# Optimization experiments

Hardware: AMD Instinct MI355X
Metric: run time of the kernel (lower is better)

The kernel has to match this reference:

```python
import jax, jax.numpy as jnp
import numpy as np

GRID = 20            # grid_size -> n1 = 400 nodes
CTX = 64             # context_size
HID = 10 * CTX       # hidden_dim per module code
BATCH = 256
K_ITERS = 100        # Dykstra iterations approximating the exact QP solve
LEAKY_SLOPE = 0.1


def _grid_incidence(g):
    """Incidence matrix of g x g grid DAG with right/down edges (SPO benchmark)."""
    n1 = g * g
    edges = []
    for i in range(g):
        for j in range(g):
            u = i * g + j
            if j + 1 < g:
                edges.append((u, u + 1))   # right
            if i + 1 < g:
                edges.append((u, u + g))   # down
    n2 = len(edges)
    A = np.zeros((n1, n2), dtype=np.float32)
    for e, (u, v) in enumerate(edges):
        A[u, e] = 1.0    # flow leaves u
        A[v, e] = -1.0   # flow enters v
    b = np.zeros(n1, dtype=np.float32)
    b[0] = 1.0           # source
    b[-1] = -1.0         # sink
    return A, b


def setup_inputs() -> dict:
    key = jax.random.key(0)
    ks = jax.random.split(key, 5)
    A_np, b_np = _grid_incidence(GRID)
    n2 = A_np.shape[1]
    d = jax.random.normal(ks[0], (BATCH, CTX), dtype=jnp.float32)
    W1 = jax.random.normal(ks[1], (CTX, HID), dtype=jnp.float32) / np.sqrt(CTX)
    b1 = jax.random.normal(ks[2], (HID,), dtype=jnp.float32) * 0.01
    W2 = jax.random.normal(ks[3], (HID, n2), dtype=jnp.float32) / np.sqrt(HID)
    b2 = jax.random.normal(ks[4], (n2,), dtype=jnp.float32) * 0.01
    return {
        "d": d, "W1": W1, "b1": b1, "W2": W2, "b2": b2,
        "A": jnp.asarray(A_np), "b_eq": jnp.asarray(b_np),
    }


def _solve_qp(w, A, b_eq):
    """Batched min_x w'x + 0.5||x||^2 s.t. Ax=b, x>=0 == proj of -w onto the
    feasible set, via Dykstra alternating projections (affine set / orthant)."""
    M = jnp.linalg.pinv(A @ A.T)  # [n1, n1]; AA' is the grid Laplacian (rank n1-1)

    def proj_affine(x):           # x: [B, n2]
        resid = x @ A.T - b_eq    # [B, n1]
        return x - (resid @ M) @ A

    y0 = -w                       # point to project
    p0 = jnp.zeros_like(w)
    q0 = jnp.zeros_like(w)

    def step(carry, _):
        y, p, q = carry
        t = y + p
        yp = proj_affine(t)
        p = t - yp
        t2 = yp + q
        y = jnp.maximum(t2, 0.0)  # projection onto x >= 0
        q = t2 - y
        return (y, p, q), None

    (y, _, _), _ = jax.lax.scan(step, (y0, p0, q0), None, length=K_ITERS)
    return y


def reference(d, W1, b1, W2, b2, A, b_eq):
    h = d @ W1 + b1
    h = jnp.where(h > 0, h, LEAKY_SLOPE * h)   # LeakyReLU(0.1)
    w = h @ W2 + b2                            # predicted edge costs [B, n2]
    return _solve_qp(w, A, b_eq)               # training-mode output: QP solution
```

## Files before the change

### kernel.cpp

```cpp
#include <hip/hip_runtime.h>
#include <math.h>

#define G 20
#define N1 400
#define N2 760
#define CTXS 64
#define HID 640
#define NB 256
#define ITERS 100
#define PI_F 3.14159265358979323846f

__device__ __forceinline__ int eR(int i, int j) { return (i < 19) ? (39 * i + 2 * j) : (741 + j); }
__device__ __forceinline__ int eD(int i, int j) { return (j < 19) ? (39 * i + 2 * j + 1) : (39 * i + 38); }

#define LOAD_ROW20(dst, base) do {                                          \
    const float4* _rp = (const float4*)(base);                              \
    float4 _r0 = _rp[0], _r1 = _rp[1], _r2 = _rp[2], _r3 = _rp[3], _r4 = _rp[4]; \
    dst[0]=_r0.x; dst[1]=_r0.y; dst[2]=_r0.z; dst[3]=_r0.w;                 \
    dst[4]=_r1.x; dst[5]=_r1.y; dst[6]=_r1.z; dst[7]=_r1.w;                 \
    dst[8]=_r2.x; dst[9]=_r2.y; dst[10]=_r2.z; dst[11]=_r2.w;               \
    dst[12]=_r3.x; dst[13]=_r3.y; dst[14]=_r3.z; dst[15]=_r3.w;             \
    dst[16]=_r4.x; dst[17]=_r4.y; dst[18]=_r4.z; dst[19]=_r4.w; } while (0)

__global__ __launch_bounds__(256, 1) void spnet_kernel(
    const float* __restrict__ dmat, const float* __restrict__ W1,
    const float* __restrict__ b1v, const float* __restrict__ W2,
    const float* __restrict__ b2v, float* __restrict__ out)
{
  const int tid = threadIdx.x;
  const int bb  = blockIdx.x;

  __shared__ __align__(16) float sdrow[CTXS];
  __shared__ __align__(16) float sh[HID];
  __shared__ __align__(16) float st0[N2];
  __shared__ __align__(16) float srowT[N1];
  __shared__ __align__(16) float sc1[N1];
  __shared__ __align__(16) float sc2T[N1];
  __shared__ __align__(16) float sd1[N1];
  __shared__ __align__(16) float szz[N1];
  __shared__ __align__(16) float tRs[G][G];
  __shared__ __align__(16) float tDs[21][G];

  for (int t = tid; t < N1; t += 256) ((float*)tRs)[t] = 0.f;
  for (int t = tid; t < 21 * G; t += 256) ((float*)tDs)[t] = 0.f;
  if (tid < CTXS) sdrow[tid] = dmat[bb * CTXS + tid];

  const bool isC = (tid < 200);
  const int c  = tid / 10;
  const int u  = tid % 10;
  const int k0 = 2 * u;

  float VA0[10], VA1[10], VC[20], S0, S1;
  {
    const float n0 = 0.22360679774997896f, nk = 0.31622776601683794f;
#pragma unroll
    for (int i = 0; i < 10; ++i) {
      VA0[i] = ((k0 == 0) ? n0 : nk) * cosf((float)(k0 * (2 * i + 1)) * (PI_F / 40.f));
      VA1[i] = nk * cosf((float)((k0 + 1) * (2 * i + 1)) * (PI_F / 40.f));
    }
#pragma unroll
    for (int k = 0; k < 20; ++k)
      VC[k] = ((k == 0) ? n0 : nk) * cosf((float)(k * (2 * u + 1)) * (PI_F / 40.f));
    float lc = 2.f - 2.f * cosf((float)c * (PI_F / 20.f));
    float l0 = 2.f - 2.f * cosf((float)k0 * (PI_F / 20.f));
    float l1 = 2.f - 2.f * cosf((float)(k0 + 1) * (PI_F / 20.f));
    S0 = (c == 0 && k0 == 0) ? 0.f : 1.f / (lc + l0);
    S1 = 1.f / (lc + l1);
  }

  __syncthreads();

  if (tid < HID / 4) {
    float4 acc = *(const float4*)(b1v + 4 * tid);
#pragma unroll 4
    for (int k = 0; k < CTXS; k += 4) {
      float4 h4 = *(const float4*)(sdrow + k);
      const float* wb = W1 + k * HID + 4 * tid;
      float4 w0 = *(const float4*)(wb);
      float4 w1 = *(const float4*)(wb + HID);
      float4 w2 = *(const float4*)(wb + 2 * HID);
      float4 w3 = *(const float4*)(wb + 3 * HID);
      acc.x = fmaf(h4.x, w0.x, acc.x); acc.y = fmaf(h4.x, w0.y, acc.y);
      acc.z = fmaf(h4.x, w0.z, acc.z); acc.w = fmaf(h4.x, w0.w, acc.w);
      acc.x = fmaf(h4.y, w1.x, acc.x); acc.y = fmaf(h4.y, w1.y, acc.y);
      acc.z = fmaf(h4.y, w1.z, acc.z); acc.w = fmaf(h4.y, w1.w, acc.w);
      acc.x = fmaf(h4.z, w2.x, acc.x); acc.y = fmaf(h4.z, w2.y, acc.y);
      acc.z = fmaf(h4.z, w2.z, acc.z); acc.w = fmaf(h4.z, w2.w, acc.w);
      acc.x = fmaf(h4.w, w3.x, acc.x); acc.y = fmaf(h4.w, w3.y, acc.y);
      acc.z = fmaf(h4.w, w3.z, acc.z); acc.w = fmaf(h4.w, w3.w, acc.w);
    }
    acc.x = acc.x > 0.f ? acc.x : 0.1f * acc.x;
    acc.y = acc.y > 0.f ? acc.y : 0.1f * acc.y;
    acc.z = acc.z > 0.f ? acc.z : 0.1f * acc.z;
    acc.w = acc.w > 0.f ? acc.w : 0.1f * acc.w;
    *(float4*)(sh + 4 * tid) = acc;
  }
  __syncthreads();

  if (tid < N2 / 4) {
    float4 acc = *(const float4*)(b2v + 4 * tid);
#pragma unroll 2
    for (int k = 0; k < HID; k += 4) {
      float4 h4 = *(const float4*)(sh + k);
      const float* wb = W2 + k * N2 + 4 * tid;
      float4 w0 = *(const float4*)(wb);
      float4 w1 = *(const float4*)(wb + N2);
      float4 w2 = *(const float4*)(wb + 2 * N2);
      float4 w3 = *(const float4*)(wb + 3 * N2);
      acc.x = fmaf(h4.x, w0.x, acc.x); acc.y = fmaf(h4.x, w0.y, acc.y);
      acc.z = fmaf(h4.x, w0.z, acc.z); acc.w = fmaf(h4.x, w0.w, acc.w);
      acc.x = fmaf(h4.y, w1.x, acc.x); acc.y = fmaf(h4.y, w1.y, acc.y);
      acc.z = fmaf(h4.y, w1.z, acc.z); acc.w = fmaf(h4.y, w1.w, acc.w);
      acc.x = fmaf(h4.z, w2.x, acc.x); acc.y = fmaf(h4.z, w2.y, acc.y);
      acc.z = fmaf(h4.z, w2.z, acc.z); acc.w = fmaf(h4.z, w2.w, acc.w);
      acc.x = fmaf(h4.w, w3.x, acc.x); acc.y = fmaf(h4.w, w3.y, acc.y);
      acc.z = fmaf(h4.w, w3.z, acc.z); acc.w = fmaf(h4.w, w3.w, acc.w);
    }
    float4 s; s.x = -acc.x; s.y = -acc.y; s.z = -acc.z; s.w = -acc.w;
    *(float4*)(st0 + 4 * tid) = s;
  }

  const int  di = tid / 5, dj4 = (tid % 5) * 4;
  const bool dAct = (tid < 100) && (di < 19);
  float dT[4], dQ[4], dY[4];
  const int  rid = tid - 128;
  const bool isR = (rid >= 0 && rid < 100);
  const int  ri = isR ? (rid / 5) : 0, rj4 = isR ? ((rid % 5) * 4) : 0;
  float rT[4], rQ[4], rY[4];
#pragma unroll
  for (int m = 0; m < 4; ++m) { dT[m]=0.f; dQ[m]=0.f; dY[m]=0.f; rT[m]=0.f; rQ[m]=0.f; rY[m]=0.f; }

  __syncthreads();

  if (dAct) {
#pragma unroll
    for (int m = 0; m < 4; ++m) dT[m] = st0[eD(di, dj4 + m)];
    *(float4*)&tDs[di + 1][dj4] = make_float4(dT[0], dT[1], dT[2], dT[3]);
  }
  if (isR) {
#pragma unroll
    for (int m = 0; m < 4; ++m) {
      int j = rj4 + m;
      rT[m] = (j < 19) ? st0[eR(ri, j)] : 0.f;
    }
    *(float4*)&tRs[ri][rj4] = make_float4(rT[0], rT[1], rT[2], rT[3]);
  }
  __syncthreads();

  for (int it = 0; it < ITERS; ++it) {
    if (isR) {
      float4 oR = *(const float4*)&tRs[ri][rj4];
      float  lf = (rj4 > 0) ? tRs[ri][rj4 - 1] : 0.f;
      float4 oD = *(const float4*)&tDs[ri + 1][rj4];
      float4 iD = *(const float4*)&tDs[ri][rj4];
      float r0 = oR.x + oD.x - lf   - iD.x;
      float r1 = oR.y + oD.y - oR.x - iD.y;
      float r2 = oR.z + oD.z - oR.y - iD.z;
      float r3 = oR.w + oD.w - oR.z - iD.w;
      if (ri == 0  && rj4 == 0)  r0 -= 1.f;
      if (ri == 19 && rj4 == 16) r3 += 1.f;
      srowT[(rj4 + 0) * G + ri] = r0;
      srowT[(rj4 + 1) * G + ri] = r1;
      srowT[(rj4 + 2) * G + ri] = r2;
      srowT[(rj4 + 3) * G + ri] = r3;
    }
    __syncthreads();

    if (isC) {
      float d_[20]; LOAD_ROW20(d_, srowT + 20 * c);
      float a0 = 0.f, a1 = 0.f;
#pragma unroll
      for (int i = 0; i < 10; ++i) {
        float e_ = d_[i] + d_[19 - i], o_ = d_[i] - d_[19 - i];
        a0 = fmaf(VA0[i], e_, a0);
        a1 = fmaf(VA1[i], o_, a1);
      }
      sc1[k0 * G + c] = a0;
      sc1[(k0 + 1) * G + c] = a1;
    }
    __syncthreads();

    if (isC) {
      float d_[20]; LOAD_ROW20(d_, sc1 + 20 * c);
      float a0 = 0.f, a1 = 0.f;
#pragma unroll
      for (int j = 0; j < 10; ++j) {
        float e_ = d_[j] + d_[19 - j], o_ = d_[j] - d_[19 - j];
        a0 = fmaf(VA0[j], e_, a0);
        a1 = fmaf(VA1[j], o_, a1);
      }
      sc2T[k0 * G + c] = a0 * S0;
      sc2T[(k0 + 1) * G + c] = a1 * S1;
    }
    __syncthreads();

    if (isC) {
      float d_[20]; LOAD_ROW20(d_, sc2T + 20 * c);
      float E = 0.f, O = 0.f;
#pragma unroll
      for (int m = 0; m < 10; ++m) {
        E = fmaf(VC[2 * m], d_[2 * m], E);
        O = fmaf(VC[2 * m + 1], d_[2 * m + 1], O);
      }
      sd1[u * G + c] = E + O;
      sd1[(19 - u) * G + c] = E - O;
    }
    __syncthreads();

    if (isC) {
      float d_[20]; LOAD_ROW20(d_, sd1 + 20 * c);
      float E = 0.f, O = 0.f;
#pragma unroll
      for (int m = 0; m < 10; ++m) {
        E = fmaf(VC[2 * m], d_[2 * m], E);
        O = fmaf(VC[2 * m + 1], d_[2 * m + 1], O);
      }
      szz[c * G + u] = E + O;
      szz[c * G + (19 - u)] = E - O;
    }
    __syncthreads();

    if (isR) {
      float4 z4 = *(const float4*)&szz[ri * G + rj4];
      float  zR = (rj4 < 16) ? szz[ri * G + rj4 + 4] : 0.f;
      float pn[4] = {z4.x - z4.y, z4.y - z4.z, z4.z - z4.w, z4.w - zR};
      if (rj4 == 16) pn[3] = 0.f;
#pragma unroll
      for (int m = 0; m < 4; ++m) {
        float t2 = rT[m] - pn[m] + rQ[m];
        float yn = fmaxf(t2, 0.f);
        rQ[m] = t2 - yn; rY[m] = yn; rT[m] = yn + pn[m];
      }
      *(float4*)&tRs[ri][rj4] = make_float4(rT[0], rT[1], rT[2], rT[3]);
    }
    if (dAct) {
      float4 z4 = *(const float4*)&szz[di * G + dj4];
      float4 zb = *(const float4*)&szz[(di + 1) * G + dj4];
      float pn[4] = {z4.x - zb.x, z4.y - zb.y, z4.z - zb.z, z4.w - zb.w};
#pragma unroll
      for (int m = 0; m < 4; ++m) {
        float t2 = dT[m] - pn[m] + dQ[m];
        float yn = fmaxf(t2, 0.f);
        dQ[m] = t2 - yn; dY[m] = yn; dT[m] = yn + pn[m];
      }
      *(float4*)&tDs[di + 1][dj4] = make_float4(dT[0], dT[1], dT[2], dT[3]);
    }
    __syncthreads();
  }

  float* mine = out + bb * N2;
  if (isR) {
#pragma unroll
    for (int m = 0; m < 4; ++m) {
      int j = rj4 + m;
      if (j < 19) mine[eR(ri, j)] = rY[m];
    }
  }
  if (dAct) {
#pragma unroll
    for (int m = 0; m < 4; ++m) mine[eD(di, dj4 + m)] = dY[m];
  }
}

extern "C" void kernel_launch(void* const* d_in, const int* in_sizes, int n_in,
                              void* d_out, int out_size, void* d_ws, size_t ws_size,
                              hipStream_t stream) {
  const float* d   = (const float*)d_in[0];
  const float* W1  = (const float*)d_in[1];
  const float* b1  = (const float*)d_in[2];
  const float* W2  = (const float*)d_in[3];
  const float* b2  = (const float*)d_in[4];
  float* out = (float*)d_out;
  spnet_kernel<<<NB, 256, 0, stream>>>(d, W1, b1, W2, b2, out);
}
```

Baseline: 214.9 us.

## Run Dykstra loop in a single wavefront without block barriers

Restricts the iterative projection loop to the first 64 threads (one wavefront on AMD) and removes all __syncthreads, relying on lockstep wave execution with compiler memory fences. Each lane now processes multiple DCT and edge-update tasks serially. DCT coefficient tables move from per-thread registers into shared memory. This trades barrier overhead for less parallelism and more per-lane work, and depends on intra-wave LDS ordering for correctness.

After: 332.5 us. +54.7%, slower.

```diff
diff --git a/kernel.cpp b/kernel.cpp
--- a/kernel.cpp
+++ b/kernel.cpp
@@ -21,6 +21,126 @@
     dst[8]=_r2.x; dst[9]=_r2.y; dst[10]=_r2.z; dst[11]=_r2.w;               \
     dst[12]=_r3.x; dst[13]=_r3.y; dst[14]=_r3.z; dst[15]=_r3.w;             \
     dst[16]=_r4.x; dst[17]=_r4.y; dst[18]=_r4.z; dst[19]=_r4.w; } while (0)
+
+#define LOAD_ROW12(dst, base) do {                                          \
+    const float4* _rp = (const float4*)(base);                              \
+    float4 _r0 = _rp[0], _r1 = _rp[1], _r2 = _rp[2];                        \
+    dst[0]=_r0.x; dst[1]=_r0.y; dst[2]=_r0.z; dst[3]=_r0.w;                 \
+    dst[4]=_r1.x; dst[5]=_r1.y; dst[6]=_r1.z; dst[7]=_r1.w;                 \
+    dst[8]=_r2.x; dst[9]=_r2.y; dst[10]=_r2.z; dst[11]=_r2.w; } while (0)
+
+#define FENCE() asm volatile("" ::: "memory")
+
+#define TASK_RESID(ri, rj4) do {                                            \
+    float4 oR = *(const float4*)&tRs[ri][rj4];                              \
+    float  lf = ((rj4) > 0) ? tRs[ri][(rj4) - 1] : 0.f;                     \
+    float4 oD = *(const float4*)&tDs[(ri) + 1][rj4];                        \
+    float4 iD = *(const float4*)&tDs[ri][rj4];                              \
+    float r0 = oR.x + oD.x - lf   - iD.x;                                   \
+    float r1 = oR.y + oD.y - oR.x - iD.y;                                   \
+    float r2 = oR.z + oD.z - oR.y - iD.z;                                   \
+    float r3 = oR.w + oD.w - oR.z - iD.w;                                   \
+    if ((ri) == 0  && (rj4) == 0)  r0 -= 1.f;                               \
+    if ((ri) == 19 && (rj4) == 16) r3 += 1.f;                               \
+    srowT[((rj4) + 0) * G + (ri)] = r0;                                     \
+    srowT[((rj4) + 1) * G + (ri)] = r1;                                     \
+    srowT[((rj4) + 2) * G + (ri)] = r2;                                     \
+    srowT[((rj4) + 3) * G + (ri)] = r3;                                     \
+  } while (0)
+
+#define TASK_A(cc, uu) do {                                                 \
+    float d_[20]; LOAD_ROW20(d_, srowT + 20 * (cc));                        \
+    float e0_[12]; LOAD_ROW12(e0_, &sVA0[uu][0]);                           \
+    float e1_[12]; LOAD_ROW12(e1_, &sVA1[uu][0]);                           \
+    float a0 = 0.f, a1 = 0.f;                                               \
+    _Pragma("unroll")                                                       \
+    for (int i = 0; i < 10; ++i) {                                          \
+      float e_ = d_[i] + d_[19 - i], o_ = d_[i] - d_[19 - i];               \
+      a0 = fmaf(e0_[i], e_, a0);                                            \
+      a1 = fmaf(e1_[i], o_, a1);                                            \
+    }                                                                       \
+    sc1[(2 * (uu)) * G + (cc)] = a0;                                        \
+    sc1[(2 * (uu) + 1) * G + (cc)] = a1;                                    \
+  } while (0)
+
+#define TASK_B(cc, uu, S0v, S1v) do {                                       \
+    float d_[20]; LOAD_ROW20(d_, sc1 + 20 * (cc));                          \
+    float e0_[12]; LOAD_ROW12(e0_, &sVA0[uu][0]);                           \
+    float e1_[12]; LOAD_ROW12(e1_, &sVA1[uu][0]);                           \
+    float a0 = 0.f, a1 = 0.f;                                               \
+    _Pragma("unroll")                                                       \
+    for (int j = 0; j < 10; ++j) {                                          \
+      float e_ = d_[j] + d_[19 - j], o_ = d_[j] - d_[19 - j];               \
+      a0 = fmaf(e0_[j], e_, a0);                                            \
+      a1 = fmaf(e1_[j], o_, a1);                                            \
+    }                                                                       \
+    sc2T[(2 * (uu)) * G + (cc)] = a0 * (S0v);                               \
+    sc2T[(2 * (uu) + 1) * G + (cc)] = a1 * (S1v);                           \
+  } while (0)
+
+#define TASK_C(cc, uu) do {                                                 \
+    float d_[20]; LOAD_ROW20(d_, sc2T + 20 * (cc));                         \
+    float vc_[20]; LOAD_ROW20(vc_, &sVC[uu][0]);                            \
+    float E = 0.f, O = 0.f;                                                 \
+    _Pragma("unroll")                                                       \
+    for (int m = 0; m < 10; ++m) {                                          \
+      E = fmaf(vc_[2 * m], d_[2 * m], E);                                   \
+      O = fmaf(vc_[2 * m + 1], d_[2 * m + 1], O);                           \
+    }                                                                       \
+    sd1[(uu) * G + (cc)] = E + O;                                           \
+    sd1[(19 - (uu)) * G + (cc)] = E - O;                                    \
+  } while (0)
+
+#define TASK_D(cc, uu) do {                                                 \
+    float d_[20]; LOAD_ROW20(d_, sd1 + 20 * (cc));                          \
+    float vc_[20]; LOAD_ROW20(vc_, &sVC[uu][0]);                            \
+    float E = 0.f, O = 0.f;                                                 \
+    _Pragma("unroll")                                                       \
+    for (int m = 0; m < 10; ++m) {                                          \
+      E = fmaf(vc_[2 * m], d_[2 * m], E);                                   \
+      O = fmaf(vc_[2 * m + 1], d_[2 * m + 1], O);                           \
+    }                                                                       \
+    szz[(cc) * G + (uu)] = E + O;                                           \
+    szz[(cc) * G + (19 - (uu))] = E - O;                                    \
+  } while (0)
+
+#define TASK_ER(ri, rj4, T, Q, Y) do {                                      \
+    float4 z4 = *(const float4*)&szz[(ri) * G + (rj4)];                     \
+    float  zR = ((rj4) < 16) ? szz[(ri) * G + (rj4) + 4] : 0.f;             \
+    float pn[4];                                                            \
+    pn[0] = z4.x - z4.y; pn[1] = z4.y - z4.z; pn[2] = z4.z - z4.w;          \
+    pn[3] = ((rj4) == 16) ? 0.f : (z4.w - zR);                              \
+    _Pragma("unroll")                                                       \
+    for (int m = 0; m < 4; ++m) {                                           \
+      float t2 = T[m] - pn[m] + Q[m];                                       \
+      float yn = fmaxf(t2, 0.f);                                            \
+      Q[m] = t2 - yn; Y[m] = yn; T[m] = yn + pn[m];                         \
+    }                                                                       \
+    *(float4*)&tRs[ri][rj4] = make_float4(T[0], T[1], T[2], T[3]);          \
+  } while (0)
+
+#define TASK_ED(di, dj4, T, Q, Y) do {                                      \
+    float4 z4 = *(const float4*)&szz[(di) * G + (dj4)];                     \
+    float4 zb = *(const float4*)&szz[((di) + 1) * G + (dj4)];               \
+    float pn[4];                                                            \
+    pn[0] = z4.x - zb.x; pn[1] = z4.y - zb.y;                               \
+    pn[2] = z4.z - zb.z; pn[3] = z4.w - zb.w;                               \
+    _Pragma("unroll")                                                       \
+    for (int m = 0; m < 4; ++m) {                                           \
+      float t2 = T[m] - pn[m] + Q[m];                                       \
+      float yn = fmaxf(t2, 0.f);                                            \
+      Q[m] = t2 - yn; Y[m] = yn; T[m] = yn + pn[m];                         \
+    }                                                                       \
+    *(float4*)&tDs[(di) + 1][dj4] = make_float4(T[0], T[1], T[2], T[3]);    \
+  } while (0)
+
+#define CALC_S(cc, uu, S0v, S1v) do {                                       \
+    float lc = 2.f - 2.f * cosf((float)(cc) * (PI_F / 20.f));               \
+    float l0 = 2.f - 2.f * cosf((float)(2 * (uu)) * (PI_F / 20.f));         \
+    float l1 = 2.f - 2.f * cosf((float)(2 * (uu) + 1) * (PI_F / 20.f));     \
+    S0v = ((cc) == 0 && (uu) == 0) ? 0.f : 1.f / (lc + l0);                 \
+    S1v = 1.f / (lc + l1);                                                  \
+  } while (0)
 
 __global__ __launch_bounds__(256, 1) void spnet_kernel(
     const float* __restrict__ dmat, const float* __restrict__ W1,
@@ -40,34 +160,28 @@
   __shared__ __align__(16) float szz[N1];
   __shared__ __align__(16) float tRs[G][G];
   __shared__ __align__(16) float tDs[21][G];
+  __shared__ __align__(16) float sVA0[10][12];
+  __shared__ __align__(16) float sVA1[10][12];
+  __shared__ __align__(16) float sVC[10][20];
 
   for (int t = tid; t < N1; t += 256) ((float*)tRs)[t] = 0.f;
   for (int t = tid; t < 21 * G; t += 256) ((float*)tDs)[t] = 0.f;
+  const float n0c = 0.22360679774997896f, nkc = 0.31622776601683794f;
+  if (tid < 120) {
+    int u = tid / 12, i = tid % 12;
+    float v0 = 0.f, v1 = 0.f;
+    if (i < 10) {
+      int k0 = 2 * u;
+      v0 = ((k0 == 0) ? n0c : nkc) * cosf((float)(k0 * (2 * i + 1)) * (PI_F / 40.f));
+      v1 = nkc * cosf((float)((k0 + 1) * (2 * i + 1)) * (PI_F / 40.f));
+    }
+    sVA0[u][i] = v0; sVA1[u][i] = v1;
+  }
+  if (tid < 200) {
+    int u = tid / 20, k = tid % 20;
+    sVC[u][k] = ((k == 0) ? n0c : nkc) * cosf((float)(k * (2 * u + 1)) * (PI_F / 40.f));
+  }
   if (tid < CTXS) sdrow[tid] = dmat[bb * CTXS + tid];
-
-  const bool isC = (tid < 200);
-  const int c  = tid / 10;
-  const int u  = tid % 10;
-  const int k0 = 2 * u;
-
-  float VA0[10], VA1[10], VC[20], S0, S1;
-  {
-    const float n0 = 0.22360679774997896f, nk = 0.31622776601683794f;
-#pragma unroll
-    for (int i = 0; i < 10; ++i) {
-      VA0[i] = ((k0 == 0) ? n0 : nk) * cosf((float)(k0 * (2 * i + 1)) * (PI_F / 40.f));
-      VA1[i] = nk * cosf((float)((k0 + 1) * (2 * i + 1)) * (PI_F / 40.f));
-    }
-#pragma unroll
-    for (int k = 0; k < 20; ++k)
-      VC[k] = ((k == 0) ? n0 : nk) * cosf((float)(k * (2 * u + 1)) * (PI_F / 40.f));
-    float lc = 2.f - 2.f * cosf((float)c * (PI_F / 20.f));
-    float l0 = 2.f - 2.f * cosf((float)k0 * (PI_F / 20.f));
-    float l1 = 2.f - 2.f * cosf((float)(k0 + 1) * (PI_F / 20.f));
-    S0 = (c == 0 && k0 == 0) ? 0.f : 1.f / (lc + l0);
-    S1 = 1.f / (lc + l1);
-  }
-
   __syncthreads();
 
   if (tid < HID / 4) {
@@ -119,146 +233,94 @@
     float4 s; s.x = -acc.x; s.y = -acc.y; s.z = -acc.z; s.w = -acc.w;
     *(float4*)(st0 + 4 * tid) = s;
   }
-
-  const int  di = tid / 5, dj4 = (tid % 5) * 4;
-  const bool dAct = (tid < 100) && (di < 19);
-  float dT[4], dQ[4], dY[4];
-  const int  rid = tid - 128;
-  const bool isR = (rid >= 0 && rid < 100);
-  const int  ri = isR ? (rid / 5) : 0, rj4 = isR ? ((rid % 5) * 4) : 0;
-  float rT[4], rQ[4], rY[4];
-#pragma unroll
-  for (int m = 0; m < 4; ++m) { dT[m]=0.f; dQ[m]=0.f; dY[m]=0.f; rT[m]=0.f; rQ[m]=0.f; rY[m]=0.f; }
-
   __syncthreads();
 
-  if (dAct) {
-#pragma unroll
-    for (int m = 0; m < 4; ++m) dT[m] = st0[eD(di, dj4 + m)];
-    *(float4*)&tDs[di + 1][dj4] = make_float4(dT[0], dT[1], dT[2], dT[3]);
-  }
-  if (isR) {
-#pragma unroll
-    for (int m = 0; m < 4; ++m) {
-      int j = rj4 + m;
-      rT[m] = (j < 19) ? st0[eR(ri, j)] : 0.f;
-    }
-    *(float4*)&tRs[ri][rj4] = make_float4(rT[0], rT[1], rT[2], rT[3]);
-  }
-  __syncthreads();
+  if (tid >= 64) return;
+  const int t = tid;
+
+  const int c0 = t / 10,         u0 = t % 10;
+  const int c1 = (t + 64) / 10,  u1 = (t + 64) % 10;
+  const int c2 = (t + 128) / 10, u2 = (t + 128) % 10;
+  const int c3 = (t + 192) / 10, u3 = (t + 192) % 10;
+  const bool a3 = (t < 8);
+  float S0_0, S1_0, S0_1, S1_1, S0_2, S1_2, S0_3, S1_3;
+  CALC_S(c0, u0, S0_0, S1_0);
+  CALC_S(c1, u1, S0_1, S1_1);
+  CALC_S(c2, u2, S0_2, S1_2);
+  CALC_S(c3, u3, S0_3, S1_3);
+
+  const int di0 = t / 5,        dj0 = (t % 5) * 4;
+  const int di1 = (t + 64) / 5, dj1 = ((t + 64) % 5) * 4;
+  const bool dA1 = (t < 31);
+  const int ri0 = t / 5,        rj0 = (t % 5) * 4;
+  const int ri1 = (t + 64) / 5, rj1 = ((t + 64) % 5) * 4;
+  const bool rA1 = (t < 36);
+
+  float dT0[4], dQ0[4], dY0[4], dT1[4], dQ1[4], dY1[4];
+  float rT0[4], rQ0[4], rY0[4], rT1[4], rQ1[4], rY1[4];
+#pragma unroll
+  for (int m = 0; m < 4; ++m) {
+    dT0[m] = 0.f; dQ0[m] = 0.f; dY0[m] = 0.f; dT1[m] = 0.f; dQ1[m] = 0.f; dY1[m] = 0.f;
+    rT0[m] = 0.f; rQ0[m] = 0.f; rY0[m] = 0.f; rT1[m] = 0.f; rQ1[m] = 0.f; rY1[m] = 0.f;
+  }
+
+  {
+#pragma unroll
+    for (int m = 0; m < 4; ++m) dT0[m] = st0[eD(di0, dj0 + m)];
+    *(float4*)&tDs[di0 + 1][dj0] = make_float4(dT0[0], dT0[1], dT0[2], dT0[3]);
+  }
+  if (dA1) {
+#pragma unroll
+    for (int m = 0; m < 4; ++m) dT1[m] = st0[eD(di1, dj1 + m)];
+    *(float4*)&tDs[di1 + 1][dj1] = make_float4(dT1[0], dT1[1], dT1[2], dT1[3]);
+  }
+  {
+#pragma unroll
+    for (int m = 0; m < 4; ++m) { int j = rj0 + m; rT0[m] = (j < 19) ? st0[eR(ri0, j)] : 0.f; }
+    *(float4*)&tRs[ri0][rj0] = make_float4(rT0[0], rT0[1], rT0[2], rT0[3]);
+  }
+  if (rA1) {
+#pragma unroll
+    for (int m = 0; m < 4; ++m) { int j = rj1 + m; rT1[m] = (j < 19) ? st0[eR(ri1, j)] : 0.f; }
+    *(float4*)&tRs[ri1][rj1] = make_float4(rT1[0], rT1[1], rT1[2], rT1[3]);
+  }
+  FENCE();
 
   for (int it = 0; it < ITERS; ++it) {
-    if (isR) {
-      float4 oR = *(const float4*)&tRs[ri][rj4];
-      float  lf = (rj4 > 0) ? tRs[ri][rj4 - 1] : 0.f;
-      float4 oD = *(const float4*)&tDs[ri + 1][rj4];
-      float4 iD = *(const float4*)&tDs[ri][rj4];
-      float r0 = oR.x + oD.x - lf   - iD.x;
-      float r1 = oR.y + oD.y - oR.x - iD.y;
-      float r2 = oR.z + oD.z - oR.y - iD.z;
-      float r3 = oR.w + oD.w - oR.z - iD.w;
-      if (ri == 0  && rj4 == 0)  r0 -= 1.f;
-      if (ri == 19 && rj4 == 16) r3 += 1.f;
-      srowT[(rj4 + 0) * G + ri] = r0;
-      srowT[(rj4 + 1) * G + ri] = r1;
-      srowT[(rj4 + 2) * G + ri] = r2;
-      srowT[(rj4 + 3) * G + ri] = r3;
-    }
-    __syncthreads();
-
-    if (isC) {
-      float d_[20]; LOAD_ROW20(d_, srowT + 20 * c);
-      float a0 = 0.f, a1 = 0.f;
-#pragma unroll
-      for (int i = 0; i < 10; ++i) {
-        float e_ = d_[i] + d_[19 - i], o_ = d_[i] - d_[19 - i];
-        a0 = fmaf(VA0[i], e_, a0);
-        a1 = fmaf(VA1[i], o_, a1);
-      }
-      sc1[k0 * G + c] = a0;
-      sc1[(k0 + 1) * G + c] = a1;
-    }
-    __syncthreads();
-
-    if (isC) {
-      float d_[20]; LOAD_ROW20(d_, sc1 + 20 * c);
-      float a0 = 0.f, a1 = 0.f;
-#pragma unroll
-      for (int j = 0; j < 10; ++j) {
-        float e_ = d_[j] + d_[19 - j], o_ = d_[j] - d_[19 - j];
-        a0 = fmaf(VA0[j], e_, a0);
-        a1 = fmaf(VA1[j], o_, a1);
-      }
-      sc2T[k0 * G + c] = a0 * S0;
-      sc2T[(k0 + 1) * G + c] = a1 * S1;
-    }
-    __syncthreads();
-
-    if (isC) {
-      float d_[20]; LOAD_ROW20(d_, sc2T + 20 * c);
-      float E = 0.f, O = 0.f;
-#pragma unroll
-      for (int m = 0; m < 10; ++m) {
-        E = fmaf(VC[2 * m], d_[2 * m], E);
-        O = fmaf(VC[2 * m + 1], d_[2 * m + 1], O);
-      }
-      sd1[u * G + c] = E + O;
-      sd1[(19 - u) * G + c] = E - O;
-    }
-    __syncthreads();
-
-    if (isC) {
-      float d_[20]; LOAD_ROW20(d_, sd1 + 20 * c);
-      float E = 0.f, O = 0.f;
-#pragma unroll
-      for (int m = 0; m < 10; ++m) {
-        E = fmaf(VC[2 * m], d_[2 * m], E);
-        O = fmaf(VC[2 * m + 1], d_[2 * m + 1], O);
-      }
-      szz[c * G + u] = E + O;
-      szz[c * G + (19 - u)] = E - O;
-    }
-    __syncthreads();
-
-    if (isR) {
-      float4 z4 = *(const float4*)&szz[ri * G + rj4];
-      float  zR = (rj4 < 16) ? szz[ri * G + rj4 + 4] : 0.f;
-      float pn[4] = {z4.x - z4.y, z4.y - z4.z, z4.z - z4.w, z4.w - zR};
-      if (rj4 == 16) pn[3] = 0.f;
-#pragma unroll
-      for (int m = 0; m < 4; ++m) {
-        float t2 = rT[m] - pn[m] + rQ[m];
-        float yn = fmaxf(t2, 0.f);
-        rQ[m] = t2 - yn; rY[m] = yn; rT[m] = yn + pn[m];
-      }
-      *(float4*)&tRs[ri][rj4] = make_float4(rT[0], rT[1], rT[2], rT[3]);
-    }
-    if (dAct) {
-      float4 z4 = *(const float4*)&szz[di * G + dj4];
-      float4 zb = *(const float4*)&szz[(di + 1) * G + dj4];
-      float pn[4] = {z4.x - zb.x, z4.y - zb.y, z4.z - zb.z, z4.w - zb.w};
-#pragma unroll
-      for (int m = 0; m < 4; ++m) {
-        float t2 = dT[m] - pn[m] + dQ[m];
-        float yn = fmaxf(t2, 0.f);
-        dQ[m] = t2 - yn; dY[m] = yn; dT[m] = yn + pn[m];
-      }
-      *(float4*)&tDs[di + 1][dj4] = make_float4(dT[0], dT[1], dT[2], dT[3]);
-    }
-    __syncthreads();
+    TASK_RESID(ri0, rj0);
+    if (rA1) TASK_RESID(ri1, rj1);
+    FENCE();
+    TASK_A(c0, u0); TASK_A(c1, u1); TASK_A(c2, u2);
+    if (a3) TASK_A(c3, u3);
+    FENCE();
+    TASK_B(c0, u0, S0_0, S1_0); TASK_B(c1, u1, S0_1, S1_1); TASK_B(c2, u2, S0_2, S1_2);
+    if (a3) TASK_B(c3, u3, S0_3, S1_3);
+    FENCE();
+    TASK_C(c0, u0); TASK_C(c1, u1); TASK_C(c2, u2);
+    if (a3) TASK_C(c3, u3);
+    FENCE();
+    TASK_D(c0, u0); TASK_D(c1, u1); TASK_D(c2, u2);
+    if (a3) TASK_D(c3, u3);
+    FENCE();
+    TASK_ER(ri0, rj0, rT0, rQ0, rY0);
+    if (rA1) TASK_ER(ri1, rj1, rT1, rQ1, rY1);
+    TASK_ED(di0, dj0, dT0, dQ0, dY0);
+    if (dA1) TASK_ED(di1, dj1, dT1, dQ1, dY1);
+    FENCE();
   }
 
   float* mine = out + bb * N2;
-  if (isR) {
-#pragma unroll
-    for (int m = 0; m < 4; ++m) {
-      int j = rj4 + m;
-      if (j < 19) mine[eR(ri, j)] = rY[m];
-    }
-  }
-  if (dAct) {
-#pragma unroll
-    for (int m = 0; m < 4; ++m) mine[eD(di, dj4 + m)] = dY[m];
+#pragma unroll
+  for (int m = 0; m < 4; ++m) { int j = rj0 + m; if (j < 19) mine[eR(ri0, j)] = rY0[m]; }
+  if (rA1) {
+#pragma unroll
+    for (int m = 0; m < 4; ++m) { int j = rj1 + m; if (j < 19) mine[eR(ri1, j)] = rY1[m]; }
+  }
+#pragma unroll
+  for (int m = 0; m < 4; ++m) mine[eD(di0, dj0 + m)] = dY0[m];
+  if (dA1) {
+#pragma unroll
+    for (int m = 0; m < 4; ++m) mine[eD(di1, dj1 + m)] = dY1[m];
   }
 }
 
```
